# Kernel tuning notes

Hardware: AMD Instinct MI355X
Metric: run time of the kernel (lower is better)

The kernel has to match this reference:

```python
import jax, jax.numpy as jnp
import numpy as np

B, C, H, W = 2, 512, 64, 64
HEADS, DHEAD = 8, 64
HID = HEADS * DHEAD  # 512
GROUPS = 32
EPS = 1e-5


def setup_inputs() -> dict:
    key = jax.random.key(0)
    ks = jax.random.split(key, 10)
    w_scale = 0.02
    return {
        "x": jax.random.normal(ks[0], (B, C, H, W), dtype=jnp.float32),
        "gamma": jnp.ones((C,), dtype=jnp.float32),
        "beta": jnp.zeros((C,), dtype=jnp.float32),
        "wq": jax.random.normal(ks[1], (HID, C), dtype=jnp.float32) * w_scale,
        "bq": jax.random.normal(ks[2], (HID,), dtype=jnp.float32) * w_scale,
        "wk": jax.random.normal(ks[3], (HID, C), dtype=jnp.float32) * w_scale,
        "bk": jax.random.normal(ks[4], (HID,), dtype=jnp.float32) * w_scale,
        "wv": jax.random.normal(ks[5], (HID, C), dtype=jnp.float32) * w_scale,
        "bv": jax.random.normal(ks[6], (HID,), dtype=jnp.float32) * w_scale,
        "wo": jax.random.normal(ks[7], (C, HID), dtype=jnp.float32) * w_scale,
        "bo": jax.random.normal(ks[8], (C,), dtype=jnp.float32) * w_scale,
    }


def _group_norm(x, gamma, beta):
    b, c, h, w = x.shape
    xg = x.reshape(b, GROUPS, c // GROUPS, h * w)
    mu = jnp.mean(xg, axis=(2, 3), keepdims=True)
    var = jnp.var(xg, axis=(2, 3), keepdims=True)
    xn = (xg - mu) * jax.lax.rsqrt(var + EPS)
    xn = xn.reshape(b, c, h, w)
    return xn * gamma[None, :, None, None] + beta[None, :, None, None]


def reference(x, gamma, beta, wq, bq, wk, bk, wv, bv, wo, bo):
    b, c, h, w = x.shape
    n = h * w
    # norm + flatten spatial; embedding=None -> self-attention on normed x
    xn = _group_norm(x, gamma, beta).reshape(b, c, n)
    # 1x1 Conv1d projections == channel matmuls
    q = jnp.einsum('oc,bcn->bon', wq, xn) + bq[None, :, None]
    k = jnp.einsum('oc,bcn->bon', wk, xn) + bk[None, :, None]
    v = jnp.einsum('oc,bcn->bon', wv, xn) + bv[None, :, None]
    scale = DHEAD ** (-0.25)  # applied to BOTH q and k, as in source
    qh = q.reshape(b, HEADS, DHEAD, n) * scale
    kh = k.reshape(b, HEADS, DHEAD, n) * scale
    vh = v.reshape(b, HEADS, DHEAD, n)
    # full NxN attention (the materialized score matrix targeted for kernel work)
    attn = jax.nn.softmax(jnp.einsum('bhdi,bhdj->bhij', qh, kh), axis=-1)
    out = jnp.einsum('bhij,bhdj->bhdi', attn, vh).reshape(b, HID, n)
    out = jnp.einsum('oc,bcn->bon', wo, out) + bo[None, :, None]
    out = out.reshape(b, c, h, w)
    return x + out  # in_channels == out_channels -> residual
```

## Files before the change

kernel.cpp:

```cpp
#include <hip/hip_runtime.h>
#include <math.h>

#define BB      2
#define CC      512
#define NN_TOK  4096
#define HEADS   8
#define DHEAD   64
#define HID     512
#define GROUPS  32
#define CPG     (CC / GROUPS)
#define EPS     1e-5f

typedef __bf16 bf16x8 __attribute__((ext_vector_type(8)));
typedef float  f32x4  __attribute__((ext_vector_type(4)));
typedef float  f32x16 __attribute__((ext_vector_type(16)));

static __device__ __forceinline__ unsigned short f2bf(float f) {
  __bf16 h = (__bf16)f;
  return __builtin_bit_cast(unsigned short, h);
}
static __device__ __forceinline__ unsigned pk_fp8x4(float a, float b, float c, float d) {
  int lo = __builtin_amdgcn_cvt_pk_fp8_f32(a, b, 0, false);
  return (unsigned)__builtin_amdgcn_cvt_pk_fp8_f32(c, d, lo, true);
}
static __device__ __forceinline__ unsigned char f2fp8(float a) {
  return (unsigned char)(__builtin_amdgcn_cvt_pk_fp8_f32(a, a, 0, false) & 0xff);
}
static __device__ __forceinline__ long mklong(unsigned lo, unsigned hi) {
  return (long)(((unsigned long long)hi << 32) | lo);
}

__global__ __launch_bounds__(256) void wconv_kernel(
    const float* __restrict__ w0, const float* __restrict__ w1,
    const float* __restrict__ w2, const float* __restrict__ w3,
    unsigned short* __restrict__ o0, unsigned short* __restrict__ o1,
    unsigned short* __restrict__ o2, unsigned short* __restrict__ o3) {
  int y = blockIdx.y;
  const float* src = (y == 0) ? w0 : (y == 1) ? w1 : (y == 2) ? w2 : w3;
  unsigned short* dst = (y == 0) ? o0 : (y == 1) ? o1 : (y == 2) ? o2 : o3;
  int idx = (blockIdx.x * 256 + threadIdx.x) * 8;
  float4 a = *(const float4*)&src[idx];
  float4 b = *(const float4*)&src[idx + 4];
  ushort4 p0, p1;
  p0.x = f2bf(a.x); p0.y = f2bf(a.y); p0.z = f2bf(a.z); p0.w = f2bf(a.w);
  p1.x = f2bf(b.x); p1.y = f2bf(b.y); p1.z = f2bf(b.z); p1.w = f2bf(b.w);
  *(ushort4*)&dst[idx] = p0;
  *(ushort4*)&dst[idx + 4] = p1;
}

__global__ __launch_bounds__(256) void gn_stats_kernel(
    const float* __restrict__ x, float2* __restrict__ part) {
  int blk = blockIdx.x;
  const float4* __restrict__ x4 = (const float4*)(x + (size_t)blk * 16384);
  int t = threadIdx.x;
  float s = 0.f, ss = 0.f;
  #pragma unroll
  for (int i = 0; i < 16; ++i) {
    float4 v = x4[t + i * 256];
    s  += v.x + v.y + v.z + v.w;
    ss += v.x * v.x + v.y * v.y + v.z * v.z + v.w * v.w;
  }
  #pragma unroll
  for (int off = 32; off >= 1; off >>= 1) {
    s  += __shfl_down(s, off, 64);
    ss += __shfl_down(ss, off, 64);
  }
  __shared__ float rs[4], rss[4];
  int wid = t >> 6, lane = t & 63;
  if (lane == 0) { rs[wid] = s; rss[wid] = ss; }
  __syncthreads();
  if (t == 0) {
    float2 o;
    o.x = rs[0] + rs[1] + rs[2] + rs[3];
    o.y = rss[0] + rss[1] + rss[2] + rss[3];
    part[blk] = o;
  }
}

__global__ __launch_bounds__(256) void gn_norm_t_kernel(
    const float* __restrict__ x, const float* __restrict__ gamma,
    const float* __restrict__ beta, const float2* __restrict__ part,
    unsigned short* __restrict__ xnT) {
  __shared__ __align__(16) unsigned short lds[64 * 72];
  __shared__ float mu4[4], rs4[4];
  int b = blockIdx.z;
  int t0 = blockIdx.x * 64, c0 = blockIdx.y * 64;
  int t = threadIdx.x;
  if (t < 4) {
    int g = (c0 >> 4) + t;
    int gi = b * GROUPS + g;
    float2 p0 = part[gi * 4 + 0], p1 = part[gi * 4 + 1];
    float2 p2 = part[gi * 4 + 2], p3 = part[gi * 4 + 3];
    float S = p0.x + p1.x + p2.x + p3.x;
    float SS = p0.y + p1.y + p2.y + p3.y;
    const float inv_n = 1.0f / (float)(CPG * NN_TOK);
    float mu = S * inv_n;
    float var = SS * inv_n - mu * mu;
    mu4[t] = mu;
    rs4[t] = rsqrtf(var + EPS);
  }
  __syncthreads();
  const float* __restrict__ xb = x + (size_t)b * CC * NN_TOK;
  #pragma unroll
  for (int i = 0; i < 4; ++i) {
    int f = t + i * 256;
    int row = f >> 4, c16 = f & 15;
    int c = c0 + row;
    float ga = gamma[c] * rs4[row >> 4];
    float be = beta[c] - mu4[row >> 4] * ga;
    float4 v = *(const float4*)&xb[(size_t)c * NN_TOK + t0 + c16 * 4];
    ushort4 pk;
    pk.x = f2bf(v.x * ga + be); pk.y = f2bf(v.y * ga + be);
    pk.z = f2bf(v.z * ga + be); pk.w = f2bf(v.w * ga + be);
    *(ushort4*)&lds[row * 72 + c16 * 4] = pk;
  }
  __syncthreads();
  unsigned short* __restrict__ ob = xnT + (size_t)b * NN_TOK * CC;
  #pragma unroll
  for (int i = 0; i < 2; ++i) {
    int f = t + i * 256;
    int row = f >> 3, ch = f & 7;
    ushort4 a, b4;
    a.x  = lds[(ch * 8 + 0) * 72 + row];
    a.y  = lds[(ch * 8 + 1) * 72 + row];
    a.z  = lds[(ch * 8 + 2) * 72 + row];
    a.w  = lds[(ch * 8 + 3) * 72 + row];
    b4.x = lds[(ch * 8 + 4) * 72 + row];
    b4.y = lds[(ch * 8 + 5) * 72 + row];
    b4.z = lds[(ch * 8 + 6) * 72 + row];
    b4.w = lds[(ch * 8 + 7) * 72 + row];
    *(ushort4*)&ob[(size_t)(t0 + row) * CC + c0 + ch * 8] = a;
    *(ushort4*)&ob[(size_t)(t0 + row) * CC + c0 + ch * 8 + 4] = b4;
  }
}

__global__ __launch_bounds__(256, 3) void qkv_gemm_kernel(
    const unsigned short* __restrict__ xnT,
    const unsigned short* __restrict__ wqb, const unsigned short* __restrict__ wkb,
    const unsigned short* __restrict__ wvb,
    const float* __restrict__ bq, const float* __restrict__ bk,
    const float* __restrict__ bv,
    unsigned char* __restrict__ qT8, unsigned char* __restrict__ kT8,
    unsigned char* __restrict__ vB8) {
  __shared__ __align__(16) unsigned short AsBs[2 * 128 * 72];
  unsigned short* As = AsBs;
  unsigned short* Bs = AsBs + 128 * 72;
  int b = blockIdx.z;
  int y = blockIdx.y;
  int which = y >> 2, yl = y & 3;
  const unsigned short* __restrict__ W =
      (which == 0) ? wqb : (which == 1) ? wkb : wvb;
  const float* __restrict__ bias = (which == 0) ? bq : (which == 1) ? bk : bv;
  int m0 = yl * 128;
  int n0 = blockIdx.x * 128;
  const unsigned short* __restrict__ Bsrc = xnT + (size_t)b * NN_TOK * CC;
  int t = threadIdx.x, w = t >> 6, lane = t & 63;
  int wm = (w >> 1) * 64, wn = (w & 1) * 64;
  int l15 = lane & 15, lq = lane >> 4;

  f32x4 acc[4][4];
  #pragma unroll
  for (int mt = 0; mt < 4; ++mt)
    #pragma unroll
    for (int nt = 0; nt < 4; ++nt) acc[mt][nt] = (f32x4){0.f, 0.f, 0.f, 0.f};

  for (int kc = 0; kc < CC; kc += 64) {
    __syncthreads();
    #pragma unroll
    for (int i = 0; i < 4; ++i) {
      int f = t + i * 256;
      int row = f >> 3, ch = f & 7;
      *(uint4*)&As[row * 72 + ch * 8] =
          *(const uint4*)&W[(size_t)(m0 + row) * CC + kc + ch * 8];
      *(uint4*)&Bs[row * 72 + ch * 8] =
          *(const uint4*)&Bsrc[(size_t)(n0 + row) * CC + kc + ch * 8];
    }
    __syncthreads();
    #pragma unroll
    for (int ks = 0; ks < 2; ++ks) {
      bf16x8 af[4], bfr[4];
      #pragma unroll
      for (int i = 0; i < 4; ++i) {
        af[i]  = *(const bf16x8*)&As[(wm + i * 16 + l15) * 72 + ks * 32 + lq * 8];
        bfr[i] = *(const bf16x8*)&Bs[(wn + i * 16 + l15) * 72 + ks * 32 + lq * 8];
      }
      #pragma unroll
      for (int mt = 0; mt < 4; ++mt)
        #pragma unroll
        for (int nt = 0; nt < 4; ++nt)
          acc[mt][nt] = __builtin_amdgcn_mfma_f32_16x16x32_bf16(
              af[mt], bfr[nt], acc[mt][nt], 0, 0, 0);
    }
  }
  __syncthreads();

  if (which < 2) {
    const float sc = (which == 0) ? 0.18033688011112043f : 1.0f;
    unsigned char* __restrict__ dstT = (which == 0) ? qT8 : kT8;
    unsigned char* buf = (unsigned char*)AsBs + w * 2304;
    int h = (m0 + wm) >> 6;
    const size_t hbase = (size_t)(b * HEADS + h) * NN_TOK;
    #pragma unroll
    for (int p = 0; p < 2; ++p) {
      #pragma unroll
      for (int mt = 0; mt < 4; ++mt) {
        float4 bv4 = *(const float4*)&bias[m0 + wm + mt * 16 + lq * 4];
        #pragma unroll
        for (int ntl = 0; ntl < 2; ++ntl) {
          int nt = p * 2 + ntl;
          f32x4 a = acc[mt][nt];
          unsigned pk = pk_fp8x4((a[0] + bv4.x) * sc, (a[1] + bv4.y) * sc,
                                 (a[2] + bv4.z) * sc, (a[3] + bv4.w) * sc);
          *(unsigned*)&buf[(ntl * 16 + l15) * 72 + mt * 16 + lq * 4] = pk;
        }
      }
      #pragma unroll
      for (int it = 0; it < 2; ++it) {
        int idx = it * 64 + lane;
        int row = idx >> 2, ch = idx & 3;
        int tok = n0 + wn + p * 32 + row;
        *(uint4*)&dstT[(hbase + tok) * DHEAD + ch * 16] =
            *(const uint4*)&buf[row * 72 + ch * 16];
      }
    }
  } else {
    unsigned char* __restrict__ dst = vB8 + (size_t)b * HID * NN_TOK;
    #pragma unroll
    for (int mt = 0; mt < 4; ++mt) {
      float4 bv4 = *(const float4*)&bias[m0 + wm + mt * 16 + lq * 4];
      float bvr[4] = {bv4.x, bv4.y, bv4.z, bv4.w};
      #pragma unroll
      for (int nt = 0; nt < 4; ++nt) {
        int tok = n0 + wn + nt * 16 + l15;
        #pragma unroll
        for (int r = 0; r < 4; ++r) {
          int m = m0 + wm + mt * 16 + lq * 4 + r;
          dst[(size_t)m * NN_TOK + tok] = f2fp8(acc[mt][nt][r] + bvr[r]);
        }
      }
    }
  }
}

__global__ __launch_bounds__(256) void outproj_kernel(
    const unsigned short* __restrict__ aoT, const unsigned short* __restrict__ wob,
    const float* __restrict__ bo, const float* __restrict__ x,
    float* __restrict__ out) {
  __shared__ __align__(16) unsigned short As[128 * 72];
  __shared__ __align__(16) unsigned short Bs[64 * 72];
  int b = blockIdx.z;
  int m0 = blockIdx.y * 128;
  int n0 = blockIdx.x * 64;
  const unsigned short* __restrict__ Bsrc = aoT + (size_t)b * NN_TOK * HID;
  int t = threadIdx.x, w = t >> 6, lane = t & 63;
  int wm = (w & 1) * 64, wn = (w >> 1) * 32;
  int l15 = lane & 15, lq = lane >> 4;

  f32x4 acc[4][2];
  #pragma unroll
  for (int mt = 0; mt < 4; ++mt)
    #pragma unroll
    for (int nt = 0; nt < 2; ++nt) acc[mt][nt] = (f32x4){0.f, 0.f, 0.f, 0.f};

  for (int kc = 0; kc < HID; kc += 64) {
    __syncthreads();
    #pragma unroll
    for (int i = 0; i < 4; ++i) {
      int f = t + i * 256;
      int row = f >> 3, ch = f & 7;
      *(uint4*)&As[row * 72 + ch * 8] =
          *(const uint4*)&wob[(size_t)(m0 + row) * HID + kc + ch * 8];
    }
    #pragma unroll
    for (int i = 0; i < 2; ++i) {
      int f = t + i * 256;
      int row = f >> 3, ch = f & 7;
      *(uint4*)&Bs[row * 72 + ch * 8] =
          *(const uint4*)&Bsrc[(size_t)(n0 + row) * HID + kc + ch * 8];
    }
    __syncthreads();
    #pragma unroll
    for (int ks = 0; ks < 2; ++ks) {
      bf16x8 af[4], bfr[2];
      #pragma unroll
      for (int i = 0; i < 4; ++i)
        af[i] = *(const bf16x8*)&As[(wm + i * 16 + l15) * 72 + ks * 32 + lq * 8];
      #pragma unroll
      for (int i = 0; i < 2; ++i)
        bfr[i] = *(const bf16x8*)&Bs[(wn + i * 16 + l15) * 72 + ks * 32 + lq * 8];
      #pragma unroll
      for (int mt = 0; mt < 4; ++mt)
        #pragma unroll
        for (int nt = 0; nt < 2; ++nt)
          acc[mt][nt] = __builtin_amdgcn_mfma_f32_16x16x32_bf16(
              af[mt], bfr[nt], acc[mt][nt], 0, 0, 0);
    }
  }

  const float* __restrict__ xb = x + (size_t)b * CC * NN_TOK;
  float* __restrict__ ob = out + (size_t)b * CC * NN_TOK;
  #pragma unroll
  for (int mt = 0; mt < 4; ++mt) {
    float4 bv4 = *(const float4*)&bo[m0 + wm + mt * 16 + lq * 4];
    float bvr[4] = {bv4.x, bv4.y, bv4.z, bv4.w};
    #pragma unroll
    for (int nt = 0; nt < 2; ++nt) {
      int tok = n0 + wn + nt * 16 + l15;
      #pragma unroll
      for (int r = 0; r < 4; ++r) {
        int m = m0 + wm + mt * 16 + lq * 4 + r;
        size_t off = (size_t)m * NN_TOK + tok;
        ob[off] = acc[mt][nt][r] + bvr[r] + xb[off];
      }
    }
  }
}

__global__ __launch_bounds__(512, 4) void attn_mfma_kernel(
    const unsigned char* __restrict__ qT8, const unsigned char* __restrict__ kT8,
    const unsigned char* __restrict__ vv8, unsigned short* __restrict__ aoT) {
  __shared__ __align__(16) unsigned char kvs[4 * 4608];
  __shared__ __align__(16) unsigned short st[4 * 2304];
  __shared__ float lbuf[128];
  unsigned char* ks8 = kvs;
  unsigned char* vs8 = kvs + 2 * 4608;
  int bh = blockIdx.y;
  int b = bh >> 3, h = bh & 7;
  int i0 = blockIdx.x * 128;
  const size_t hb = (size_t)bh * NN_TOK;
  const unsigned char* __restrict__ qtg = qT8 + hb * DHEAD;
  const unsigned char* __restrict__ ktg = kT8 + hb * DHEAD;
  const unsigned char* __restrict__ vg  = vv8 + hb * DHEAD;
  int t = threadIdx.x;
  int w = t >> 6, lane = t & 63, l31 = lane & 31, q1h = lane >> 5;
  int strip = w & 3, parity = w >> 2;
  int iw = i0 + strip * 32;

  const unsigned char* qrow = qtg + (size_t)(iw + l31) * DHEAD;
  uint4 qv0 = *(const uint4*)(qrow);
  uint4 qv1 = *(const uint4*)(qrow + 16);
  uint4 qv2 = *(const uint4*)(qrow + 32);
  uint4 qv3 = *(const uint4*)(qrow + 48);
  long qf[4];
  qf[0] = q1h ? mklong(qv0.z, qv0.w) : mklong(qv0.x, qv0.y);
  qf[1] = q1h ? mklong(qv1.z, qv1.w) : mklong(qv1.x, qv1.y);
  qf[2] = q1h ? mklong(qv2.z, qv2.w) : mklong(qv2.x, qv2.y);
  qf[3] = q1h ? mklong(qv3.z, qv3.w) : mklong(qv3.x, qv3.y);

  f32x16 o0 = {0,0,0,0,0,0,0,0,0,0,0,0,0,0,0,0};
  f32x16 o1 = {0,0,0,0,0,0,0,0,0,0,0,0,0,0,0,0};
  float lrun = 0.f;
  const unsigned char* __restrict__ ksw = ks8 + parity * 4608;
  const unsigned char* __restrict__ vsw = vs8 + parity * 4608;

  for (int rt = 0; rt < NN_TOK / 128; ++rt) {
    int j0 = rt * 128;
    __syncthreads();
    {
      int jr = t >> 2, ch = t & 3;
      int ktile = jr >> 6, krow = jr & 63;
      uint4 kx = *(const uint4*)&ktg[(size_t)(j0 + jr) * DHEAD + ch * 16];
      unsigned char* kd = &ks8[ktile * 4608 + krow * 72 + ch * 16];
      *(uint2*)kd = make_uint2(kx.x, kx.y);
      *(uint2*)(kd + 8) = make_uint2(kx.z, kx.w);
      int vtile = t >> 8, vrr = (t >> 2) & 63, vch = t & 3;
      uint4 vx = *(const uint4*)&vg[(size_t)vrr * NN_TOK + j0 + vtile * 64 + vch * 16];
      unsigned char* vd = &vs8[vtile * 4608 + vrr * 72 + vch * 16];
      *(uint2*)vd = make_uint2(vx.x, vx.y);
      *(uint2*)(vd + 8) = make_uint2(vx.z, vx.w);
    }
    __syncthreads();

    f32x16 s0 = {0,0,0,0,0,0,0,0,0,0,0,0,0,0,0,0};
    f32x16 s1 = {0,0,0,0,0,0,0,0,0,0,0,0,0,0,0,0};
    #pragma unroll
    for (int s = 0; s < 4; ++s) {
      long a0 = *(const long*)&ksw[l31 * 72 + s * 16 + q1h * 8];
      long a1 = *(const long*)&ksw[(32 + l31) * 72 + s * 16 + q1h * 8];
      s0 = __builtin_amdgcn_mfma_f32_32x32x16_fp8_fp8(a0, qf[s], s0, 0, 0, 0);
      s1 = __builtin_amdgcn_mfma_f32_32x32x16_fp8_fp8(a1, qf[s], s1, 0, 0, 0);
    }

    unsigned pk4[8];
    float psum = 0.f;
    #pragma unroll
    for (int g = 0; g < 4; ++g) {
      float p0 = __builtin_amdgcn_exp2f(s0[4 * g + 0]);
      float p1 = __builtin_amdgcn_exp2f(s0[4 * g + 1]);
      float p2 = __builtin_amdgcn_exp2f(s0[4 * g + 2]);
      float p3 = __builtin_amdgcn_exp2f(s0[4 * g + 3]);
      psum += (p0 + p1) + (p2 + p3);
      pk4[g] = pk_fp8x4(p0, p1, p2, p3);
    }
    #pragma unroll
    for (int g = 0; g < 4; ++g) {
      float p0 = __builtin_amdgcn_exp2f(s1[4 * g + 0]);
      float p1 = __builtin_amdgcn_exp2f(s1[4 * g + 1]);
      float p2 = __builtin_amdgcn_exp2f(s1[4 * g + 2]);
      float p3 = __builtin_amdgcn_exp2f(s1[4 * g + 3]);
      psum += (p0 + p1) + (p2 + p3);
      pk4[4 + g] = pk_fp8x4(p0, p1, p2, p3);
    }
    psum += __shfl_xor(psum, 32);
    lrun += psum;

    #pragma unroll
    for (int s = 0; s < 4; ++s) {
      long va0 = *(const long*)&vsw[l31 * 72 + s * 16 + q1h * 8];
      long va1 = *(const long*)&vsw[(32 + l31) * 72 + s * 16 + q1h * 8];
      unsigned own_lo = pk4[2 * s], own_hi = pk4[2 * s + 1];
      unsigned send = q1h ? own_lo : own_hi;
      unsigned got = (unsigned)__shfl_xor((int)send, 32);
      unsigned lo = q1h ? got : own_lo;
      unsigned hi = q1h ? own_hi : got;
      long pb = mklong(lo, hi);
      o0 = __builtin_amdgcn_mfma_f32_32x32x16_fp8_fp8(va0, pb, o0, 0, 0, 0);
      o1 = __builtin_amdgcn_mfma_f32_32x32x16_fp8_fp8(va1, pb, o1, 0, 0, 0);
    }
  }

  float* obuf = (float*)kvs;
  __syncthreads();
  if (parity == 1) {
    #pragma unroll
    for (int r = 0; r < 16; ++r) {
      int d = (r & 3) + 8 * (r >> 2) + 4 * q1h;
      obuf[strip * 1024 + d * 32 + l31] = o0[r];
    }
    if (q1h == 0) lbuf[strip * 32 + l31] = lrun;
  }
  __syncthreads();
  if (parity == 0) {
    lrun += lbuf[strip * 32 + l31];
    #pragma unroll
    for (int r = 0; r < 16; ++r) {
      int d = (r & 3) + 8 * (r >> 2) + 4 * q1h;
      o0[r] += obuf[strip * 1024 + d * 32 + l31];
    }
  }
  __syncthreads();
  if (parity == 1) {
    #pragma unroll
    for (int r = 0; r < 16; ++r) {
      int d = (r & 3) + 8 * (r >> 2) + 4 * q1h;
      obuf[strip * 1024 + d * 32 + l31] = o1[r];
    }
  }
  __syncthreads();
  if (parity == 0) {
    #pragma unroll
    for (int r = 0; r < 16; ++r) {
      int d = (r & 3) + 8 * (r >> 2) + 4 * q1h;
      o1[r] += obuf[strip * 1024 + d * 32 + l31];
    }
    float inv = 1.0f / lrun;
    unsigned short* stw = st + strip * 2304;
    #pragma unroll
    for (int dm = 0; dm < 2; ++dm) {
      #pragma unroll
      for (int g = 0; g < 4; ++g) {
        float v[4];
        #pragma unroll
        for (int i = 0; i < 4; ++i) {
          int r = 4 * g + i;
          v[i] = ((dm == 0) ? o0[r] : o1[r]) * inv;
        }
        ushort4 pk;
        pk.x = f2bf(v[0]); pk.y = f2bf(v[1]); pk.z = f2bf(v[2]); pk.w = f2bf(v[3]);
        *(ushort4*)&stw[l31 * 72 + dm * 32 + g * 8 + q1h * 4] = pk;
      }
    }
    const size_t obase = (size_t)b * NN_TOK;
    #pragma unroll
    for (int it = 0; it < 4; ++it) {
      int idx = it * 64 + lane;
      int row = idx >> 3, ch = idx & 7;
      int tok = iw + row;
      *(uint4*)&aoT[(obase + tok) * HID + h * DHEAD + ch * 8] =
          *(const uint4*)&stw[row * 72 + ch * 8];
    }
  }
}

extern "C" void kernel_launch(void* const* d_in, const int* in_sizes, int n_in,
                              void* d_out, int out_size, void* d_ws, size_t ws_size,
                              hipStream_t stream) {
  const float* x     = (const float*)d_in[0];
  const float* gamma = (const float*)d_in[1];
  const float* beta  = (const float*)d_in[2];
  const float* wq    = (const float*)d_in[3];
  const float* bq    = (const float*)d_in[4];
  const float* wk    = (const float*)d_in[5];
  const float* bk    = (const float*)d_in[6];
  const float* wv    = (const float*)d_in[7];
  const float* bv    = (const float*)d_in[8];
  const float* wo    = (const float*)d_in[9];
  const float* bo    = (const float*)d_in[10];
  float* out = (float*)d_out;

  const size_t SZ = (size_t)BB * CC * NN_TOK;
  const size_t WZ = (size_t)CC * HID;
  unsigned short* xnT = (unsigned short*)d_ws;
  unsigned char*  qT8 = (unsigned char*)(xnT + SZ);
  unsigned char*  kT8 = qT8 + SZ;
  unsigned char*  vB8 = kT8 + SZ;
  unsigned short* aoT = (unsigned short*)(vB8 + SZ);
  unsigned short* wqb = aoT + SZ;
  unsigned short* wkb = wqb + WZ;
  unsigned short* wvb = wkb + WZ;
  unsigned short* wob = wvb + WZ;
  float2* gnpart = (float2*)(wob + WZ);

  wconv_kernel<<<dim3(128, 4), dim3(256), 0, stream>>>(
      wq, wk, wv, wo, wqb, wkb, wvb, wob);

  gn_stats_kernel<<<dim3(256), dim3(256), 0, stream>>>(x, gnpart);
  gn_norm_t_kernel<<<dim3(NN_TOK / 64, CC / 64, BB), dim3(256), 0, stream>>>(
      x, gamma, beta, gnpart, xnT);

  qkv_gemm_kernel<<<dim3(NN_TOK / 128, 12, BB), dim3(256), 0, stream>>>(
      xnT, wqb, wkb, wvb, bq, bk, bv, qT8, kT8, vB8);

  attn_mfma_kernel<<<dim3(NN_TOK / 128, BB * HEADS), dim3(512), 0, stream>>>(
      qT8, kT8, vB8, aoT);

  outproj_kernel<<<dim3(NN_TOK / 64, CC / 128, BB), dim3(256), 0, stream>>>(
      aoT, wob, bo, x, out);
}
```

Measured before the change: 197.4 us.

## Split attention over two key halves with combine kernel, FP8 out-projection, fuse weight conversion

The attention kernel now splits the key/value range into two halves, doubling the grid. Each half writes unnormalized bf16 partial outputs and row sums, and a new combine kernel adds them, normalizes and emits FP8 activations. The output projection switches from bf16 MFMA to FP8 MFMA, with the weights pre-scaled by 16 and descaled in the epilogue. Weight conversion is folded into the group-norm stats kernel, and the QKV epilogue staging buffer gets a new padding plus an extra barrier. The goal is more parallelism in attention and less traffic in the projection, at the cost of extra partial-buffer traffic, one more launch and lower FP8 precision; the combine is only correct if both halves share a softmax offset.

Measured after the change: 205.7 us. 4.2% more time.

```diff
diff --git a/kernel.cpp b/kernel.cpp
--- a/kernel.cpp
+++ b/kernel.cpp
@@ -19,6 +19,10 @@
   __bf16 h = (__bf16)f;
   return __builtin_bit_cast(unsigned short, h);
 }
+static __device__ __forceinline__ float bf2f(unsigned short u) {
+  unsigned v = (unsigned)u << 16;
+  return __builtin_bit_cast(float, v);
+}
 static __device__ __forceinline__ unsigned pk_fp8x4(float a, float b, float c, float d) {
   int lo = __builtin_amdgcn_cvt_pk_fp8_f32(a, b, 0, false);
   return (unsigned)__builtin_amdgcn_cvt_pk_fp8_f32(c, d, lo, true);
@@ -29,30 +33,42 @@
 static __device__ __forceinline__ long mklong(unsigned lo, unsigned hi) {
   return (long)(((unsigned long long)hi << 32) | lo);
 }
-
-__global__ __launch_bounds__(256) void wconv_kernel(
-    const float* __restrict__ w0, const float* __restrict__ w1,
-    const float* __restrict__ w2, const float* __restrict__ w3,
-    unsigned short* __restrict__ o0, unsigned short* __restrict__ o1,
-    unsigned short* __restrict__ o2, unsigned short* __restrict__ o3) {
-  int y = blockIdx.y;
-  const float* src = (y == 0) ? w0 : (y == 1) ? w1 : (y == 2) ? w2 : w3;
-  unsigned short* dst = (y == 0) ? o0 : (y == 1) ? o1 : (y == 2) ? o2 : o3;
-  int idx = (blockIdx.x * 256 + threadIdx.x) * 8;
-  float4 a = *(const float4*)&src[idx];
-  float4 b = *(const float4*)&src[idx + 4];
-  ushort4 p0, p1;
-  p0.x = f2bf(a.x); p0.y = f2bf(a.y); p0.z = f2bf(a.z); p0.w = f2bf(a.w);
-  p1.x = f2bf(b.x); p1.y = f2bf(b.y); p1.z = f2bf(b.z); p1.w = f2bf(b.w);
-  *(ushort4*)&dst[idx] = p0;
-  *(ushort4*)&dst[idx + 4] = p1;
-}
-
-__global__ __launch_bounds__(256) void gn_stats_kernel(
-    const float* __restrict__ x, float2* __restrict__ part) {
+#define WSCALE 16.0f
+#define WSCALE_INV 0.0625f
+
+__global__ __launch_bounds__(256) void gn_stats_wconv_kernel(
+    const float* __restrict__ x, float2* __restrict__ part,
+    const float* __restrict__ wq, const float* __restrict__ wk,
+    const float* __restrict__ wv, const float* __restrict__ wo,
+    unsigned short* __restrict__ wqb, unsigned short* __restrict__ wkb,
+    unsigned short* __restrict__ wvb, unsigned char* __restrict__ wo8) {
   int blk = blockIdx.x;
+  int t = threadIdx.x;
+  {
+    int base = blk * 4096 + t * 16;
+    if (blk < 192) {
+      int wsel = base >> 18;
+      int off = base & 262143;
+      const float* s = (wsel == 0) ? wq : (wsel == 1) ? wk : wv;
+      unsigned short* d = (wsel == 0) ? wqb : (wsel == 1) ? wkb : wvb;
+      #pragma unroll
+      for (int i = 0; i < 4; ++i) {
+        float4 a = *(const float4*)&s[off + i * 4];
+        ushort4 p;
+        p.x = f2bf(a.x); p.y = f2bf(a.y); p.z = f2bf(a.z); p.w = f2bf(a.w);
+        *(ushort4*)&d[off + i * 4] = p;
+      }
+    } else {
+      int off = base - 786432;
+      #pragma unroll
+      for (int i = 0; i < 4; ++i) {
+        float4 a = *(const float4*)&wo[off + i * 4];
+        *(unsigned*)&wo8[off + i * 4] =
+            pk_fp8x4(a.x * WSCALE, a.y * WSCALE, a.z * WSCALE, a.w * WSCALE);
+      }
+    }
+  }
   const float4* __restrict__ x4 = (const float4*)(x + (size_t)blk * 16384);
-  int t = threadIdx.x;
   float s = 0.f, ss = 0.f;
   #pragma unroll
   for (int i = 0; i < 16; ++i) {
@@ -197,7 +213,7 @@
   if (which < 2) {
     const float sc = (which == 0) ? 0.18033688011112043f : 1.0f;
     unsigned char* __restrict__ dstT = (which == 0) ? qT8 : kT8;
-    unsigned char* buf = (unsigned char*)AsBs + w * 2304;
+    unsigned char* buf = (unsigned char*)AsBs + w * 2560;
     int h = (m0 + wm) >> 6;
     const size_t hbase = (size_t)(b * HEADS + h) * NN_TOK;
     #pragma unroll
@@ -211,7 +227,7 @@
           f32x4 a = acc[mt][nt];
           unsigned pk = pk_fp8x4((a[0] + bv4.x) * sc, (a[1] + bv4.y) * sc,
                                  (a[2] + bv4.z) * sc, (a[3] + bv4.w) * sc);
-          *(unsigned*)&buf[(ntl * 16 + l15) * 72 + mt * 16 + lq * 4] = pk;
+          *(unsigned*)&buf[(ntl * 16 + l15) * 80 + mt * 16 + lq * 4] = pk;
         }
       }
       #pragma unroll
@@ -220,8 +236,9 @@
         int row = idx >> 2, ch = idx & 3;
         int tok = n0 + wn + p * 32 + row;
         *(uint4*)&dstT[(hbase + tok) * DHEAD + ch * 16] =
-            *(const uint4*)&buf[row * 72 + ch * 16];
-      }
+            *(const uint4*)&buf[row * 80 + ch * 16];
+      }
+      __syncthreads();
     }
   } else {
     unsigned char* __restrict__ dst = vB8 + (size_t)b * HID * NN_TOK;
@@ -243,15 +260,15 @@
 }
 
 __global__ __launch_bounds__(256) void outproj_kernel(
-    const unsigned short* __restrict__ aoT, const unsigned short* __restrict__ wob,
+    const unsigned char* __restrict__ aoT8, const unsigned char* __restrict__ wo8,
     const float* __restrict__ bo, const float* __restrict__ x,
     float* __restrict__ out) {
-  __shared__ __align__(16) unsigned short As[128 * 72];
-  __shared__ __align__(16) unsigned short Bs[64 * 72];
+  __shared__ __align__(16) unsigned char As8[128 * 80];
+  __shared__ __align__(16) unsigned char Bs8[64 * 80];
   int b = blockIdx.z;
   int m0 = blockIdx.y * 128;
   int n0 = blockIdx.x * 64;
-  const unsigned short* __restrict__ Bsrc = aoT + (size_t)b * NN_TOK * HID;
+  const unsigned char* __restrict__ Bsrc = aoT8 + (size_t)b * NN_TOK * HID;
   int t = threadIdx.x, w = t >> 6, lane = t & 63;
   int wm = (w & 1) * 64, wn = (w >> 1) * 32;
   int l15 = lane & 15, lq = lane >> 4;
@@ -265,34 +282,32 @@
   for (int kc = 0; kc < HID; kc += 64) {
     __syncthreads();
     #pragma unroll
-    for (int i = 0; i < 4; ++i) {
-      int f = t + i * 256;
-      int row = f >> 3, ch = f & 7;
-      *(uint4*)&As[row * 72 + ch * 8] =
-          *(const uint4*)&wob[(size_t)(m0 + row) * HID + kc + ch * 8];
-    }
-    #pragma unroll
     for (int i = 0; i < 2; ++i) {
       int f = t + i * 256;
-      int row = f >> 3, ch = f & 7;
-      *(uint4*)&Bs[row * 72 + ch * 8] =
-          *(const uint4*)&Bsrc[(size_t)(n0 + row) * HID + kc + ch * 8];
+      int row = f >> 2, ch = f & 3;
+      *(uint4*)&As8[row * 80 + ch * 16] =
+          *(const uint4*)&wo8[(size_t)(m0 + row) * HID + kc + ch * 16];
+    }
+    {
+      int row = t >> 2, ch = t & 3;
+      *(uint4*)&Bs8[row * 80 + ch * 16] =
+          *(const uint4*)&Bsrc[(size_t)(n0 + row) * HID + kc + ch * 16];
     }
     __syncthreads();
     #pragma unroll
     for (int ks = 0; ks < 2; ++ks) {
-      bf16x8 af[4], bfr[2];
+      long af[4], bfr[2];
       #pragma unroll
       for (int i = 0; i < 4; ++i)
-        af[i] = *(const bf16x8*)&As[(wm + i * 16 + l15) * 72 + ks * 32 + lq * 8];
+        af[i] = *(const long*)&As8[(wm + i * 16 + l15) * 80 + ks * 32 + lq * 8];
       #pragma unroll
       for (int i = 0; i < 2; ++i)
-        bfr[i] = *(const bf16x8*)&Bs[(wn + i * 16 + l15) * 72 + ks * 32 + lq * 8];
+        bfr[i] = *(const long*)&Bs8[(wn + i * 16 + l15) * 80 + ks * 32 + lq * 8];
       #pragma unroll
       for (int mt = 0; mt < 4; ++mt)
         #pragma unroll
         for (int nt = 0; nt < 2; ++nt)
-          acc[mt][nt] = __builtin_amdgcn_mfma_f32_16x16x32_bf16(
+          acc[mt][nt] = __builtin_amdgcn_mfma_f32_16x16x32_fp8_fp8(
               af[mt], bfr[nt], acc[mt][nt], 0, 0, 0);
     }
   }
@@ -310,7 +325,7 @@
       for (int r = 0; r < 4; ++r) {
         int m = m0 + wm + mt * 16 + lq * 4 + r;
         size_t off = (size_t)m * NN_TOK + tok;
-        ob[off] = acc[mt][nt][r] + bvr[r] + xb[off];
+        ob[off] = acc[mt][nt][r] * WSCALE_INV + bvr[r] + xb[off];
       }
     }
   }
@@ -318,14 +333,15 @@
 
 __global__ __launch_bounds__(512, 4) void attn_mfma_kernel(
     const unsigned char* __restrict__ qT8, const unsigned char* __restrict__ kT8,
-    const unsigned char* __restrict__ vv8, unsigned short* __restrict__ aoT) {
+    const unsigned char* __restrict__ vv8,
+    unsigned short* __restrict__ Pp, float* __restrict__ Lp) {
   __shared__ __align__(16) unsigned char kvs[4 * 4608];
   __shared__ __align__(16) unsigned short st[4 * 2304];
   __shared__ float lbuf[128];
   unsigned char* ks8 = kvs;
   unsigned char* vs8 = kvs + 2 * 4608;
-  int bh = blockIdx.y;
-  int b = bh >> 3, h = bh & 7;
+  int by = blockIdx.y;
+  int bh = by >> 1, jhalf = by & 1;
   int i0 = blockIdx.x * 128;
   const size_t hb = (size_t)bh * NN_TOK;
   const unsigned char* __restrict__ qtg = qT8 + hb * DHEAD;
@@ -353,7 +369,7 @@
   const unsigned char* __restrict__ ksw = ks8 + parity * 4608;
   const unsigned char* __restrict__ vsw = vs8 + parity * 4608;
 
-  for (int rt = 0; rt < NN_TOK / 128; ++rt) {
+  for (int rt = jhalf * 16; rt < jhalf * 16 + 16; ++rt) {
     int j0 = rt * 128;
     __syncthreads();
     {
@@ -453,32 +469,62 @@
       int d = (r & 3) + 8 * (r >> 2) + 4 * q1h;
       o1[r] += obuf[strip * 1024 + d * 32 + l31];
     }
-    float inv = 1.0f / lrun;
     unsigned short* stw = st + strip * 2304;
     #pragma unroll
     for (int dm = 0; dm < 2; ++dm) {
       #pragma unroll
       for (int g = 0; g < 4; ++g) {
-        float v[4];
-        #pragma unroll
-        for (int i = 0; i < 4; ++i) {
-          int r = 4 * g + i;
-          v[i] = ((dm == 0) ? o0[r] : o1[r]) * inv;
-        }
         ushort4 pk;
-        pk.x = f2bf(v[0]); pk.y = f2bf(v[1]); pk.z = f2bf(v[2]); pk.w = f2bf(v[3]);
+        float v0 = (dm == 0) ? o0[4 * g + 0] : o1[4 * g + 0];
+        float v1 = (dm == 0) ? o0[4 * g + 1] : o1[4 * g + 1];
+        float v2 = (dm == 0) ? o0[4 * g + 2] : o1[4 * g + 2];
+        float v3 = (dm == 0) ? o0[4 * g + 3] : o1[4 * g + 3];
+        pk.x = f2bf(v0); pk.y = f2bf(v1); pk.z = f2bf(v2); pk.w = f2bf(v3);
         *(ushort4*)&stw[l31 * 72 + dm * 32 + g * 8 + q1h * 4] = pk;
       }
     }
-    const size_t obase = (size_t)b * NN_TOK;
+    int slot = jhalf * 16 + bh;
+    if (q1h == 0) Lp[(size_t)slot * NN_TOK + iw + l31] = lrun;
+    unsigned short* __restrict__ Ppg = Pp + (size_t)slot * NN_TOK * DHEAD;
     #pragma unroll
     for (int it = 0; it < 4; ++it) {
       int idx = it * 64 + lane;
       int row = idx >> 3, ch = idx & 7;
       int tok = iw + row;
-      *(uint4*)&aoT[(obase + tok) * HID + h * DHEAD + ch * 8] =
+      *(uint4*)&Ppg[(size_t)tok * DHEAD + ch * 8] =
           *(const uint4*)&stw[row * 72 + ch * 8];
     }
+  }
+}
+
+__global__ __launch_bounds__(256) void attn_combine_kernel(
+    const unsigned short* __restrict__ Pp, const float* __restrict__ Lp,
+    unsigned char* __restrict__ aoT8) {
+  int bh = blockIdx.y;
+  int b = bh >> 3, h = bh & 7;
+  int t0 = blockIdx.x * 64;
+  int t = threadIdx.x;
+  const unsigned short* __restrict__ A = Pp + (size_t)bh * NN_TOK * DHEAD;
+  const unsigned short* __restrict__ B = Pp + (size_t)(16 + bh) * NN_TOK * DHEAD;
+  const float* __restrict__ la = Lp + (size_t)bh * NN_TOK;
+  const float* __restrict__ lb = Lp + (size_t)(16 + bh) * NN_TOK;
+  #pragma unroll
+  for (int it = 0; it < 2; ++it) {
+    int f = t + it * 256;
+    int row = f >> 3, ch = f & 7;
+    int tok = t0 + row;
+    float inv = 1.0f / (la[tok] + lb[tok]);
+    uint4 av = *(const uint4*)&A[(size_t)tok * DHEAD + ch * 8];
+    uint4 bv = *(const uint4*)&B[(size_t)tok * DHEAD + ch * 8];
+    const unsigned short* ap = (const unsigned short*)&av;
+    const unsigned short* bp = (const unsigned short*)&bv;
+    float o[8];
+    #pragma unroll
+    for (int j = 0; j < 8; ++j) o[j] = (bf2f(ap[j]) + bf2f(bp[j])) * inv;
+    unsigned lo = pk_fp8x4(o[0], o[1], o[2], o[3]);
+    unsigned hi = pk_fp8x4(o[4], o[5], o[6], o[7]);
+    *(uint2*)&aoT8[((size_t)(b * NN_TOK + tok)) * HID + h * DHEAD + ch * 8] =
+        make_uint2(lo, hi);
   }
 }
 
@@ -504,26 +550,30 @@
   unsigned char*  qT8 = (unsigned char*)(xnT + SZ);
   unsigned char*  kT8 = qT8 + SZ;
   unsigned char*  vB8 = kT8 + SZ;
-  unsigned short* aoT = (unsigned short*)(vB8 + SZ);
-  unsigned short* wqb = aoT + SZ;
+  unsigned char*  aoT8 = vB8 + SZ;
+  unsigned short* wqb = (unsigned short*)(aoT8 + SZ);
   unsigned short* wkb = wqb + WZ;
   unsigned short* wvb = wkb + WZ;
-  unsigned short* wob = wvb + WZ;
-  float2* gnpart = (float2*)(wob + WZ);
-
-  wconv_kernel<<<dim3(128, 4), dim3(256), 0, stream>>>(
-      wq, wk, wv, wo, wqb, wkb, wvb, wob);
-
-  gn_stats_kernel<<<dim3(256), dim3(256), 0, stream>>>(x, gnpart);
+  unsigned char*  wo8 = (unsigned char*)(wvb + WZ);
+  float2* gnpart = (float2*)(wo8 + WZ);
+  unsigned short* Pp = (unsigned short*)(gnpart + 256);
+  float* Lp = (float*)(Pp + (size_t)32 * NN_TOK * DHEAD);
+
+  gn_stats_wconv_kernel<<<dim3(256), dim3(256), 0, stream>>>(
+      x, gnpart, wq, wk, wv, wo, wqb, wkb, wvb, wo8);
+
   gn_norm_t_kernel<<<dim3(NN_TOK / 64, CC / 64, BB), dim3(256), 0, stream>>>(
       x, gamma, beta, gnpart, xnT);
 
   qkv_gemm_kernel<<<dim3(NN_TOK / 128, 12, BB), dim3(256), 0, stream>>>(
       xnT, wqb, wkb, wvb, bq, bk, bv, qT8, kT8, vB8);
 
-  attn_mfma_kernel<<<dim3(NN_TOK / 128, BB * HEADS), dim3(512), 0, stream>>>(
-      qT8, kT8, vB8, aoT);
+  attn_mfma_kernel<<<dim3(NN_TOK / 128, BB * HEADS * 2), dim3(512), 0, stream>>>(
+      qT8, kT8, vB8, Pp, Lp);
+
+  attn_combine_kernel<<<dim3(NN_TOK / 64, BB * HEADS), dim3(256), 0, stream>>>(
+      Pp, Lp, aoT8);
 
   outproj_kernel<<<dim3(NN_TOK / 64, CC / 128, BB), dim3(256), 0, stream>>>(
-      aoT, wob, bo, x, out);
-}
+      aoT8, wo8, bo, x, out);
+}
```
